# Kernel tuning notes

Measured on AMD Instinct MI355X. Metric: run time of the kernel, lower is better.

Reference implementation:

```python
import jax, jax.numpy as jnp
import numpy as np

D_MODEL = 768
NUM_HEADS = 12
HEAD_DIM = D_MODEL // NUM_HEADS  # 64, also rotary dim
INTERMEDIATE = 1152
WINDOW = 128          # config.local_attention (layer_id=1 -> local layer)
ROPE_BASE = 10000.0   # local_rope_theta
EPS = 1e-5


def layer_norm_nocenter(x, gamma):
    # keras LayerNormalization(center=False): mean-subtract, no beta
    mu = jnp.mean(x, axis=-1, keepdims=True)
    var = jnp.var(x, axis=-1, keepdims=True)
    return (x - mu) * jax.lax.rsqrt(var + EPS) * gamma


def rotate_half(x):
    x1, x2 = jnp.split(x, 2, axis=-1)
    return jnp.concatenate([-x2, x1], axis=-1)


def setup_inputs() -> dict:
    key = jax.random.key(0)
    ks = jax.random.split(key, 7)
    B, S = 4, 2048
    hidden_states = jax.random.normal(ks[0], (B, S, D_MODEL), dtype=jnp.float32)
    attention_mask = jnp.zeros((B, 1, S, S), dtype=jnp.float32)  # no padding
    s = 0.02
    attn_norm_gamma = jnp.ones((D_MODEL,), dtype=jnp.float32)
    wqkv = jax.random.normal(ks[1], (D_MODEL, 3 * D_MODEL), dtype=jnp.float32) * s
    wo_attn = jax.random.normal(ks[2], (D_MODEL, D_MODEL), dtype=jnp.float32) * s
    mlp_norm_gamma = jnp.ones((D_MODEL,), dtype=jnp.float32)
    wi = jax.random.normal(ks[3], (D_MODEL, 2 * INTERMEDIATE), dtype=jnp.float32) * s
    wo_mlp = jax.random.normal(ks[4], (INTERMEDIATE, D_MODEL), dtype=jnp.float32) * s
    return {
        'hidden_states': hidden_states,
        'attention_mask': attention_mask,
        'attn_norm_gamma': attn_norm_gamma,
        'wqkv': wqkv,
        'wo_attn': wo_attn,
        'mlp_norm_gamma': mlp_norm_gamma,
        'wi': wi,
        'wo_mlp': wo_mlp,
    }


def reference(hidden_states, attention_mask, attn_norm_gamma, wqkv, wo_attn,
              mlp_norm_gamma, wi, wo_mlp):
    B, S, Dm = hidden_states.shape
    H, Dh = NUM_HEADS, HEAD_DIM

    # RoPE cache (NTKScaling with scaling_factor=1 -> plain RoPE)
    idx = jnp.arange(0, Dh, 2, dtype=jnp.float32)
    inv_freq = 1.0 / (ROPE_BASE ** (idx / Dh))          # [Dh/2]
    t = jnp.arange(S, dtype=jnp.float32)
    freqs = t[:, None] * inv_freq[None, :]              # [S, Dh/2]
    emb = jnp.concatenate([freqs, freqs], axis=-1)      # [S, Dh]
    cos = jnp.cos(emb)[None, None]                      # [1,1,S,Dh]
    sin = jnp.sin(emb)[None, None]

    # combined sliding-window + padding mask
    pos = jnp.arange(S)
    dist = jnp.abs(pos[:, None] - pos[None, :])
    neg = jnp.finfo(jnp.float32).min
    local = jnp.where(dist <= WINDOW // 2, 0.0, neg).astype(jnp.float32)
    mask = attention_mask + local[None, None]           # [B,1,S,S]

    # attention (layer_id != 0 -> pre-norm)
    x = layer_norm_nocenter(hidden_states, attn_norm_gamma)
    qkv = (x @ wqkv).reshape(B, S, 3, H, Dh).transpose(2, 0, 3, 1, 4)
    q, k, v = qkv[0], qkv[1], qkv[2]                    # [B,H,S,Dh]
    q = q * cos + rotate_half(q) * sin
    k = k * cos + rotate_half(k) * sin

    scale = 1.0 / jnp.sqrt(jnp.asarray(Dh, q.dtype))
    scores = jnp.einsum('bhqd,bhkd->bhqk', q, k) * scale + mask
    attn = jax.nn.softmax(scores, axis=-1)
    ctx = jnp.einsum('bhqk,bhkd->bhqd', attn, v)
    attn_out = ctx.transpose(0, 2, 1, 3).reshape(B, S, Dm) @ wo_attn

    h = hidden_states + attn_out

    # GLU MLP: Wi -> split -> gelu(x)*gate -> Wo, residual
    n = layer_norm_nocenter(h, mlp_norm_gamma)
    x_in, gate = jnp.split(n @ wi, 2, axis=-1)
    mlp = jax.nn.gelu(x_in, approximate=False) * gate
    return h + mlp @ wo_mlp
```

## Files before the change

kernel.cpp:

```cpp
#include <hip/hip_runtime.h>
#include <cstdint>
#include <cstddef>

typedef __bf16 bf16;
typedef float f32x4 __attribute__((ext_vector_type(4)));
typedef __bf16 bf16x8 __attribute__((ext_vector_type(8)));
typedef __bf16 bf16x4 __attribute__((ext_vector_type(4)));
typedef __bf16 bf16x2 __attribute__((ext_vector_type(2)));

#define MFMA16(a, b, c) __builtin_amdgcn_mfma_f32_16x16x32_bf16((a), (b), (c), 0, 0, 0)

__device__ __forceinline__ void gload_lds16(const void* g, void* l) {
  __builtin_amdgcn_global_load_lds((__attribute__((address_space(1))) void*)g,
                                   (__attribute__((address_space(3))) void*)l,
                                   16, 0, 0);
}

__global__ __launch_bounds__(256) void wconv_ln(const float* __restrict__ wqkv,
                                                const float* __restrict__ woa,
                                                const float* __restrict__ wi,
                                                const float* __restrict__ wom,
                                                bf16* __restrict__ wqkvT,
                                                bf16* __restrict__ woaT,
                                                bf16* __restrict__ wiT,
                                                bf16* __restrict__ womT,
                                                const float* __restrict__ X,
                                                const float* __restrict__ gamma,
                                                bf16* __restrict__ xnout) {
  __shared__ float tile[32][33];
  const int t = threadIdx.x;
  int id = blockIdx.x;
  if (id >= 4896) {
    const int row = id - 4896;
    const float* xr = X + (size_t)row * 768;
    float v0 = xr[t], v1 = xr[t + 256], v2 = xr[t + 512];
    float s = v0 + v1 + v2;
    float s2 = v0 * v0 + v1 * v1 + v2 * v2;
#pragma unroll
    for (int m = 1; m <= 32; m <<= 1) {
      s += __shfl_xor(s, m, 64);
      s2 += __shfl_xor(s2, m, 64);
    }
    float* red = &tile[0][0];
    const int w = t >> 6, lane = t & 63;
    if (lane == 0) { red[w] = s; red[4 + w] = s2; }
    __syncthreads();
    s = red[0] + red[1] + red[2] + red[3];
    s2 = red[4] + red[5] + red[6] + red[7];
    const float mu = s * (1.f / 768.f);
    const float var = s2 * (1.f / 768.f) - mu * mu;
    const float rs = rsqrtf(var + 1e-5f);
    xnout[(size_t)row * 768 + t] = (bf16)((v0 - mu) * rs * gamma[t]);
    xnout[(size_t)row * 768 + t + 256] = (bf16)((v1 - mu) * rs * gamma[t + 256]);
    xnout[(size_t)row * 768 + t + 512] = (bf16)((v2 - mu) * rs * gamma[t + 512]);
    return;
  }
  const float* W;
  bf16* Wt;
  int K, N, bx, by;
  if (id < 1728) { W = wqkv; Wt = wqkvT; K = 768; N = 2304; bx = id % 72; by = id / 72; }
  else if (id < 2304) { id -= 1728; W = woa; Wt = woaT; K = 768; N = 768; bx = id % 24; by = id / 24; }
  else if (id < 4032) { id -= 2304; W = wi; Wt = wiT; K = 768; N = 2304; bx = id % 72; by = id / 72; }
  else { id -= 4032; W = wom; Wt = womT; K = 1152; N = 768; bx = id % 24; by = id / 24; }
  const int n0 = bx * 32, k0 = by * 32;
  const int c = t & 31, r = t >> 5;
#pragma unroll
  for (int i = 0; i < 4; ++i)
    tile[r + i * 8][c] = W[(size_t)(k0 + r + i * 8) * N + n0 + c];
  __syncthreads();
#pragma unroll
  for (int i = 0; i < 4; ++i)
    Wt[(size_t)(n0 + r + i * 8) * K + k0 + c] = (bf16)tile[c][r + i * 8];
}

__global__ __launch_bounds__(256) void ln_kernel(const float* __restrict__ X,
                                                 const float* __restrict__ gamma,
                                                 bf16* __restrict__ out) {
  const int row = blockIdx.x, t = threadIdx.x;
  const float* xr = X + (size_t)row * 768;
  float v0 = xr[t], v1 = xr[t + 256], v2 = xr[t + 512];
  float s = v0 + v1 + v2;
  float s2 = v0 * v0 + v1 * v1 + v2 * v2;
#pragma unroll
  for (int m = 1; m <= 32; m <<= 1) {
    s += __shfl_xor(s, m, 64);
    s2 += __shfl_xor(s2, m, 64);
  }
  __shared__ float red[8];
  const int w = t >> 6, lane = t & 63;
  if (lane == 0) { red[w] = s; red[4 + w] = s2; }
  __syncthreads();
  s = red[0] + red[1] + red[2] + red[3];
  s2 = red[4] + red[5] + red[6] + red[7];
  const float mu = s * (1.f / 768.f);
  const float var = s2 * (1.f / 768.f) - mu * mu;
  const float rs = rsqrtf(var + 1e-5f);
  out[(size_t)row * 768 + t] = (bf16)((v0 - mu) * rs * gamma[t]);
  out[(size_t)row * 768 + t + 256] = (bf16)((v1 - mu) * rs * gamma[t + 256]);
  out[(size_t)row * 768 + t + 512] = (bf16)((v2 - mu) * rs * gamma[t + 512]);
}

template <int BM, bool RES, typename TOUT>
__global__ __launch_bounds__(256) void gemm_bt(const bf16* __restrict__ A,
                                               const bf16* __restrict__ Bt,
                                               const float* __restrict__ Res,
                                               TOUT* __restrict__ C, int M, int N, int K) {
  constexpr int MT = BM / 32;
  __shared__ __align__(16) bf16 As[BM * 64];
  __shared__ __align__(16) bf16 Bs[128 * 64];
  const int t = threadIdx.x;
  const int lane = t & 63;
  const int w = t >> 6;
  const int wm = w >> 1, wn = w & 1;
  const int row0 = blockIdx.x * BM, col0 = blockIdx.y * 128;
  const int rm = lane & 15, qd = lane >> 4;
  f32x4 acc[MT][4] = {};
  for (int k0 = 0; k0 < K; k0 += 64) {
#pragma unroll
    for (int i = 0; i < BM / 32; ++i) {
      int c = i * 256 + t;
      int r = c >> 3, j = (c & 7) ^ (r & 7);
      gload_lds16(A + (size_t)(row0 + r) * K + (k0 + j * 8), &As[c * 8]);
    }
#pragma unroll
    for (int i = 0; i < 4; ++i) {
      int c = i * 256 + t;
      int r = c >> 3, j = (c & 7) ^ (r & 7);
      gload_lds16(Bt + (size_t)(col0 + r) * K + (k0 + j * 8), &Bs[c * 8]);
    }
    __syncthreads();
#pragma unroll
    for (int kb = 0; kb < 2; ++kb) {
      bf16x8 af[MT], bfr[4];
#pragma unroll
      for (int mt = 0; mt < MT; ++mt) {
        int r = wm * (MT * 16) + mt * 16 + rm;
        af[mt] = *(const bf16x8*)&As[r * 64 + (((kb * 4 + qd) ^ (r & 7)) * 8)];
      }
#pragma unroll
      for (int nt = 0; nt < 4; ++nt) {
        int r = wn * 64 + nt * 16 + rm;
        bfr[nt] = *(const bf16x8*)&Bs[r * 64 + (((kb * 4 + qd) ^ (r & 7)) * 8)];
      }
#pragma unroll
      for (int mt = 0; mt < MT; ++mt)
#pragma unroll
        for (int nt = 0; nt < 4; ++nt)
          acc[mt][nt] = MFMA16(af[mt], bfr[nt], acc[mt][nt]);
    }
    __syncthreads();
  }
#pragma unroll
  for (int mt = 0; mt < MT; ++mt)
#pragma unroll
    for (int nt = 0; nt < 4; ++nt) {
      const int gc = col0 + wn * 64 + nt * 16 + rm;
#pragma unroll
      for (int r = 0; r < 4; ++r) {
        const int gr = row0 + wm * (MT * 16) + mt * 16 + qd * 4 + r;
        float v = acc[mt][nt][r];
        const size_t idx = (size_t)gr * N + gc;
        if (RES) v += Res[idx];
        C[idx] = (TOUT)v;
      }
    }
}

__global__ __launch_bounds__(256) void gemm_qkv(const bf16* __restrict__ A,
                                                const bf16* __restrict__ Bt,
                                                bf16* __restrict__ Qb,
                                                bf16* __restrict__ Kb,
                                                bf16* __restrict__ Vt) {
  __shared__ __align__(16) bf16 SM[17408];
  bf16* As = SM;
  bf16* Bs = SM + 8192;

  const int t = threadIdx.x;
  const int lane = t & 63;
  const int w = t >> 6;
  const int wm = w >> 1, wn = w & 1;
  const int row0 = blockIdx.x * 128, col0 = blockIdx.y * 128;
  const int rm = lane & 15, qd = lane >> 4;
  f32x4 acc[4][4] = {};
  for (int k0 = 0; k0 < 768; k0 += 64) {
#pragma unroll
    for (int i = 0; i < 4; ++i) {
      int c = i * 256 + t;
      int r = c >> 3, j = (c & 7) ^ (r & 7);
      gload_lds16(A + (size_t)(row0 + r) * 768 + (k0 + j * 8), &As[c * 8]);
      gload_lds16(Bt + (size_t)(col0 + r) * 768 + (k0 + j * 8), &Bs[c * 8]);
    }
    __syncthreads();
#pragma unroll
    for (int kb = 0; kb < 2; ++kb) {
      bf16x8 af[4], bfr[4];
#pragma unroll
      for (int mt = 0; mt < 4; ++mt) {
        int r = wm * 64 + mt * 16 + rm;
        af[mt] = *(const bf16x8*)&As[r * 64 + (((kb * 4 + qd) ^ (r & 7)) * 8)];
      }
#pragma unroll
      for (int nt = 0; nt < 4; ++nt) {
        int r = wn * 64 + nt * 16 + rm;
        bfr[nt] = *(const bf16x8*)&Bs[r * 64 + (((kb * 4 + qd) ^ (r & 7)) * 8)];
      }
#pragma unroll
      for (int mt = 0; mt < 4; ++mt)
#pragma unroll
        for (int nt = 0; nt < 4; ++nt)
          acc[mt][nt] = MFMA16(af[mt], bfr[nt], acc[mt][nt]);
    }
    __syncthreads();
  }

  const int head_id = blockIdx.y * 2 + wn;
  const int typ = blockIdx.y / 6;
  const int b = row0 >> 11;
  const int sblk = row0 & 2047;
  const int sw = sblk + wm * 64;

  if (typ < 2) {
    const int h = head_id - typ * 12;
    const size_t bhbase = (size_t)(b * 12 + h) * 2048;
    bf16* dst = typ ? Kb : Qb;
    constexpr float inv2pi = 0.15915494309189535f;
#pragma unroll
    for (int nt = 0; nt < 2; ++nt) {
      const int d = nt * 16 + rm;
      const float invf = exp2f((float)d * -0.41524101186092029f);
      float rev = (float)(sw + qd * 4) * invf * inv2pi;
      rev -= floorf(rev);
      float cs = __builtin_amdgcn_cosf(rev);
      float sn = __builtin_amdgcn_sinf(rev);
      float rv1 = invf * inv2pi;
      float c1 = __builtin_amdgcn_cosf(rv1), s1 = __builtin_amdgcn_sinf(rv1);
      float rv13 = 13.f * invf * inv2pi;
      rv13 -= floorf(rv13);
      float c13 = __builtin_amdgcn_cosf(rv13), s13 = __builtin_amdgcn_sinf(rv13);
#pragma unroll
      for (int mt = 0; mt < 4; ++mt)
#pragma unroll
        for (int r = 0; r < 4; ++r) {
          const int s = sw + mt * 16 + qd * 4 + r;
          const float x1 = acc[mt][nt][r], x2 = acc[mt][nt + 2][r];
          bf16x2 v2;
          v2[0] = (bf16)(x1 * cs - x2 * sn);
          v2[1] = (bf16)(x2 * cs + x1 * sn);
          *(bf16x2*)&dst[(bhbase + s) * 64 + 2 * d] = v2;
          const float ca = (r < 3) ? c1 : c13, sa = (r < 3) ? s1 : s13;
          const float cn = cs * ca - sn * sa;
          sn = sn * ca + cs * sa;
          cs = cn;
        }
    }
  } else {
#pragma unroll
    for (int mt = 0; mt < 4; ++mt)
#pragma unroll
      for (int nt = 0; nt < 4; ++nt) {
        int hd = wn * 64 + nt * 16 + rm;
        int sl = wm * 64 + mt * 16 + qd * 4;
        bf16x4 v4;
#pragma unroll
        for (int r = 0; r < 4; ++r) v4[r] = (bf16)acc[mt][nt][r];
        *(bf16x4*)&SM[hd * 136 + sl] = v4;
      }
    __syncthreads();
    const int h0 = blockIdx.y * 2 - 24;
#pragma unroll
    for (int it = 0; it < 8; ++it) {
      int cc = it * 256 + t;
      int hd = cc >> 4, s8 = (cc & 15) * 8;
      bf16x8 vv = *(const bf16x8*)&SM[hd * 136 + s8];
      size_t grow = (size_t)(b * 12 + h0 + (hd >> 6)) * 64 + (hd & 63);
      *(bf16x8*)&Vt[grow * 2048 + sblk + s8] = vv;
    }
  }
}

__global__ __launch_bounds__(256) void attn_kernel(const bf16* __restrict__ Qb,
                                                   const bf16* __restrict__ Kb,
                                                   const bf16* __restrict__ Vt,
                                                   const float* __restrict__ am,
                                                   bf16* __restrict__ ctx) {
  __shared__ __align__(16) bf16 KP[64 * 200];
  __shared__ __align__(16) bf16 Vts[64 * 192];
  bf16* Ks = KP;
  bf16* Ps = KP;

  const int t = threadIdx.x;
  const int lane = t & 63, w = t >> 6;
  const int rm = lane & 15, qd = lane >> 4;
  const int s0 = blockIdx.x * 64;
  const int bh = blockIdx.y;
  const int b = bh / 12, h = bh - b * 12;
  const size_t baseQ = (size_t)bh * 2048;

#pragma unroll
  for (int i = 0; i < 6; ++i) {
    int c = i * 256 + t;
    int r = c >> 3, j = (c & 7) ^ (r & 7);
    int key = min(max(s0 - 64 + r, 0), 2047);
    gload_lds16(Kb + (baseQ + key) * 64 + j * 8, &Ks[c * 8]);
  }
#pragma unroll
  for (int i = 0; i < 6; ++i) {
    int c = i * 256 + t;
    int r = c / 24, jl = c - r * 24;
    int j = (jl & 24) | ((jl & 7) ^ (r & 7));
    int k0 = min(max(s0 - 64 + j * 8, 0), 2040);
    gload_lds16(Vt + ((size_t)bh * 64 + r) * 2048 + k0, &Vts[c * 8]);
  }

  bf16x8 aq[2];
#pragma unroll
  for (int kb = 0; kb < 2; ++kb)
    aq[kb] = *(const bf16x8*)&Qb[(baseQ + s0 + w * 16 + rm) * 64 + kb * 32 + qd * 8];

  float msk[12][4];
#pragma unroll
  for (int nt = 0; nt < 12; ++nt) {
    int key = s0 - 64 + nt * 16 + rm;
#pragma unroll
    for (int r = 0; r < 4; ++r) {
      int qpos = s0 + w * 16 + qd * 4 + r;
      bool valid = (key >= 0) && (key < 2048) && (key - qpos <= 64) && (qpos - key <= 64);
      msk[nt][r] = valid ? am[((size_t)b * 2048 + qpos) * 2048 + key] : -3e38f;
    }
  }
  __syncthreads();

  f32x4 sc[12];
#pragma unroll
  for (int nt = 0; nt < 12; ++nt) {
    f32x4 a = {0.f, 0.f, 0.f, 0.f};
#pragma unroll
    for (int kb = 0; kb < 2; ++kb) {
      int r = nt * 16 + rm;
      bf16x8 bk = *(const bf16x8*)&Ks[r * 64 + (((kb * 4 + qd) ^ (rm & 7)) * 8)];
      a = MFMA16(aq[kb], bk, a);
    }
    sc[nt] = a;
  }

  float mx[4] = {-3e38f, -3e38f, -3e38f, -3e38f};
#pragma unroll
  for (int nt = 0; nt < 12; ++nt)
#pragma unroll
    for (int r = 0; r < 4; ++r) {
      float v = (msk[nt][r] <= -2.9e38f) ? -3e38f : sc[nt][r] * 0.125f + msk[nt][r];
      sc[nt][r] = v;
      mx[r] = fmaxf(mx[r], v);
    }
#pragma unroll
  for (int r = 0; r < 4; ++r)
#pragma unroll
    for (int m = 1; m <= 8; m <<= 1) mx[r] = fmaxf(mx[r], __shfl_xor(mx[r], m, 64));
  float sum[4] = {0.f, 0.f, 0.f, 0.f};
#pragma unroll
  for (int nt = 0; nt < 12; ++nt)
#pragma unroll
    for (int r = 0; r < 4; ++r) {
      float p = (sc[nt][r] > -1e37f) ? __expf(sc[nt][r] - mx[r]) : 0.f;
      sc[nt][r] = p;
      sum[r] += p;
    }
#pragma unroll
  for (int r = 0; r < 4; ++r)
#pragma unroll
    for (int m = 1; m <= 8; m <<= 1) sum[r] += __shfl_xor(sum[r], m, 64);
  float inv[4];
#pragma unroll
  for (int r = 0; r < 4; ++r) inv[r] = 1.f / sum[r];

  __syncthreads();

#pragma unroll
  for (int nt = 0; nt < 12; ++nt)
#pragma unroll
    for (int r = 0; r < 4; ++r)
      Ps[(w * 16 + qd * 4 + r) * 200 + nt * 16 + rm] = (bf16)(sc[nt][r] * inv[r]);

  f32x4 o[4] = {};
#pragma unroll
  for (int ks = 0; ks < 6; ++ks) {
    bf16x8 ap = *(const bf16x8*)&Ps[(w * 16 + rm) * 200 + ks * 32 + qd * 8];
#pragma unroll
    for (int nt = 0; nt < 4; ++nt) {
      int kc = ks * 4 + qd;
      bf16x8 bv = *(const bf16x8*)&Vts[(nt * 16 + rm) * 192 +
                                       (((kc & 24) | ((kc & 7) ^ (rm & 7))) * 8)];
      o[nt] = MFMA16(ap, bv, o[nt]);
    }
  }
#pragma unroll
  for (int nt = 0; nt < 4; ++nt)
#pragma unroll
    for (int r = 0; r < 4; ++r) {
      int q_ = s0 + w * 16 + qd * 4 + r;
      ctx[((size_t)(b * 2048 + q_)) * 768 + h * 64 + nt * 16 + rm] = (bf16)o[nt][r];
    }
}

__global__ __launch_bounds__(128) void geglu_kernel(const bf16* __restrict__ X,
                                                    bf16* __restrict__ out) {
  const int row = blockIdx.y;
  const int c = blockIdx.x * 128 + threadIdx.x;
  const bf16* xr = X + (size_t)row * 2304;
  float x = (float)xr[c], g = (float)xr[1152 + c];
  float ge = 0.5f * x * (1.0f + erff(x * 0.70710678118654752f));
  out[(size_t)row * 1152 + c] = (bf16)(ge * g);
}

extern "C" void kernel_launch(void* const* d_in, const int* in_sizes, int n_in,
                              void* d_out, int out_size, void* d_ws, size_t ws_size,
                              hipStream_t stream) {
  (void)in_sizes; (void)n_in; (void)out_size; (void)ws_size;
  const float* hidden = (const float*)d_in[0];
  const float* amask = (const float*)d_in[1];
  const float* g1 = (const float*)d_in[2];
  const float* wqkv = (const float*)d_in[3];
  const float* woa = (const float*)d_in[4];
  const float* g2 = (const float*)d_in[5];
  const float* wi = (const float*)d_in[6];
  const float* wom = (const float*)d_in[7];
  float* out = (float*)d_out;

  char* p = (char*)d_ws;
  size_t o = 0;
  auto take = [&](size_t bytes) {
    char* r = p + o;
    o = (o + bytes + 255) & ~(size_t)255;
    return r;
  };
  bf16* wqkvT = (bf16*)take((size_t)2304 * 768 * 2);
  bf16* woaT = (bf16*)take((size_t)768 * 768 * 2);
  bf16* wiT = (bf16*)take((size_t)2304 * 768 * 2);
  bf16* womT = (bf16*)take((size_t)768 * 1152 * 2);
  bf16* xn = (bf16*)take((size_t)8192 * 768 * 2);
  bf16* Qb = (bf16*)take((size_t)98304 * 64 * 2);
  bf16* Kb = (bf16*)take((size_t)98304 * 64 * 2);
  bf16* Vt = (bf16*)take((size_t)98304 * 64 * 2);
  bf16* ctxb = (bf16*)take((size_t)8192 * 768 * 2);
  float* hbuf = (float*)take((size_t)8192 * 768 * 4);
  bf16* mlpx = (bf16*)take((size_t)8192 * 2304 * 2);
  bf16* mlp = (bf16*)take((size_t)8192 * 1152 * 2);

  wconv_ln<<<13088, 256, 0, stream>>>(wqkv, woa, wi, wom, wqkvT, woaT, wiT, womT,
                                      hidden, g1, xn);

  gemm_qkv<<<dim3(64, 18), 256, 0, stream>>>(xn, wqkvT, Qb, Kb, Vt);
  attn_kernel<<<dim3(32, 48), 256, 0, stream>>>(Qb, Kb, Vt, amask, ctxb);
  gemm_bt<64, true, float><<<dim3(128, 6), 256, 0, stream>>>(ctxb, woaT, hidden, hbuf,
                                                             8192, 768, 768);

  ln_kernel<<<8192, 256, 0, stream>>>(hbuf, g2, xn);
  gemm_bt<128, false, bf16><<<dim3(64, 18), 256, 0, stream>>>(xn, wiT, nullptr, mlpx,
                                                              8192, 2304, 768);
  geglu_kernel<<<dim3(9, 8192), 128, 0, stream>>>(mlpx, mlp);
  gemm_bt<64, true, float><<<dim3(128, 6), 256, 0, stream>>>(mlp, womT, hbuf, out,
                                                             8192, 768, 1152);
}
```

Measured before the change: 326.4 us.

## Double-buffer GEMMs with 256-row tiles and fuse GEGLU into Wi GEMM epilogue

All GEMMs move to 512-thread blocks with 256x128 tiles and a double-buffered LDS pipeline that prefetches the next k-tiles with async global-to-LDS loads while MFMAs run, using explicit waitcnt, barriers and setprio. The Wi GEMM interleaves the x and gate weight rows so each block holds matching columns, applying GELU*gate in the epilogue and removing the separate geglu kernel and its intermediate buffer. The goal is to hide load latency and cut memory traffic. The cost is higher LDS use per block, fewer blocks for the narrow GEMMs (192 blocks), and hand-counted vmcnt values that must stay correct.

```diff
diff --git a/kernel.cpp b/kernel.cpp
--- a/kernel.cpp
+++ b/kernel.cpp
@@ -100,121 +100,155 @@
   out[(size_t)row * 768 + t + 512] = (bf16)((v2 - mu) * rs * gamma[t + 512]);
 }
 
-template <int BM, bool RES, typename TOUT>
-__global__ __launch_bounds__(256) void gemm_bt(const bf16* __restrict__ A,
-                                               const bf16* __restrict__ Bt,
-                                               const float* __restrict__ Res,
-                                               TOUT* __restrict__ C, int M, int N, int K) {
-  constexpr int MT = BM / 32;
-  __shared__ __align__(16) bf16 As[BM * 64];
-  __shared__ __align__(16) bf16 Bs[128 * 64];
+#define GEMM_CORE_LOOP(NT_, AROW_EXPR, BROW_EXPR)                                   \
+  auto stage = [&](int tile) {                                                      \
+    const int kk0 = tile * 64;                                                      \
+    bf16* Ab_ = &SM[(tile & 1) * 24576];                                            \
+    bf16* Bb_ = Ab_ + 16384;                                                        \
+    _Pragma("unroll") for (int i = 0; i < 4; ++i) {                                 \
+      int c = i * 512 + t;                                                          \
+      int r = c >> 3, j = (c & 7) ^ (r & 7);                                        \
+      gload_lds16(Ap + (size_t)(AROW_EXPR) * Kd + (kk0 + j * 8), &Ab_[c * 8]);      \
+    }                                                                               \
+    _Pragma("unroll") for (int i = 0; i < 2; ++i) {                                 \
+      int c = i * 512 + t;                                                          \
+      int r = c >> 3, j = (c & 7) ^ (r & 7);                                        \
+      gload_lds16(Bp + (size_t)(BROW_EXPR) * Kd + (kk0 + j * 8), &Bb_[c * 8]);      \
+    }                                                                               \
+  };                                                                                \
+  stage(0);                                                                         \
+  stage(1);                                                                         \
+  asm volatile("s_waitcnt vmcnt(6)" ::: "memory");                                  \
+  __builtin_amdgcn_s_barrier();                                                     \
+  __builtin_amdgcn_sched_barrier(0);                                                \
+  for (int tt = 0; tt < NT_; ++tt) {                                                \
+    const bf16* Ab = &SM[(tt & 1) * 24576];                                         \
+    const bf16* Bb = Ab + 16384;                                                    \
+    bf16x8 af[4], bfr[4];                                                           \
+                                                                \
+    _Pragma("unroll") for (int mt = 0; mt < 4; ++mt) {                              \
+      int r = wm * 64 + mt * 16 + rm;                                               \
+      af[mt] = *(const bf16x8*)&Ab[r * 64 + ((qd ^ (r & 7)) * 8)];                  \
+    }                                                                               \
+    _Pragma("unroll") for (int nt = 0; nt < 4; ++nt) {                              \
+      int r = wn * 64 + nt * 16 + rm;                                               \
+      bfr[nt] = *(const bf16x8*)&Bb[r * 64 + ((qd ^ (r & 7)) * 8)];                 \
+    }                                                                               \
+    __builtin_amdgcn_s_barrier();                                                   \
+    __builtin_amdgcn_sched_barrier(0);                                              \
+    __builtin_amdgcn_s_setprio(1);                                                  \
+    _Pragma("unroll") for (int mt = 0; mt < 4; ++mt)                                \
+        _Pragma("unroll") for (int nt = 0; nt < 4; ++nt)                            \
+            acc[mt][nt] = MFMA16(af[mt], bfr[nt], acc[mt][nt]);                     \
+    __builtin_amdgcn_s_setprio(0);                                                  \
+    __builtin_amdgcn_s_barrier();                                                   \
+    __builtin_amdgcn_sched_barrier(0);                                              \
+                                                                \
+    _Pragma("unroll") for (int mt = 0; mt < 4; ++mt) {                              \
+      int r = wm * 64 + mt * 16 + rm;                                               \
+      af[mt] = *(const bf16x8*)&Ab[r * 64 + (((4 + qd) ^ (r & 7)) * 8)];            \
+    }                                                                               \
+    _Pragma("unroll") for (int nt = 0; nt < 4; ++nt) {                              \
+      int r = wn * 64 + nt * 16 + rm;                                               \
+      bfr[nt] = *(const bf16x8*)&Bb[r * 64 + (((4 + qd) ^ (r & 7)) * 8)];           \
+    }                                                                               \
+    asm volatile("s_waitcnt lgkmcnt(0)" ::: "memory");                              \
+    __builtin_amdgcn_sched_barrier(0);                                              \
+    __builtin_amdgcn_s_barrier();           \
+    __builtin_amdgcn_sched_barrier(0);                                              \
+    if (tt + 2 < NT_) stage(tt + 2);                                                \
+    __builtin_amdgcn_s_setprio(1);                                                  \
+    _Pragma("unroll") for (int mt = 0; mt < 4; ++mt)                                \
+        _Pragma("unroll") for (int nt = 0; nt < 4; ++nt)                            \
+            acc[mt][nt] = MFMA16(af[mt], bfr[nt], acc[mt][nt]);                     \
+    __builtin_amdgcn_s_setprio(0);                                                  \
+    if (tt + 2 < NT_) {                                                             \
+      asm volatile("s_waitcnt vmcnt(6)" ::: "memory");                              \
+    } else {                                                                        \
+      asm volatile("s_waitcnt vmcnt(0)" ::: "memory");                              \
+    }                                                                               \
+    __builtin_amdgcn_s_barrier();                                                   \
+    __builtin_amdgcn_sched_barrier(0);                                              \
+  }
+
+template <int EPI, int NT>
+__global__ __launch_bounds__(512, 2) void gemm_big(const bf16* __restrict__ Ap,
+                                                   const bf16* __restrict__ Bp,
+                                                   const float* __restrict__ Res,
+                                                   void* __restrict__ Cout,
+                                                   int Nout) {
+  constexpr int Kd = NT * 64;
+  __shared__ __align__(16) bf16 SM[49152];
   const int t = threadIdx.x;
-  const int lane = t & 63;
-  const int w = t >> 6;
+  const int lane = t & 63, w = t >> 6;
   const int wm = w >> 1, wn = w & 1;
-  const int row0 = blockIdx.x * BM, col0 = blockIdx.y * 128;
   const int rm = lane & 15, qd = lane >> 4;
-  f32x4 acc[MT][4] = {};
-  for (int k0 = 0; k0 < K; k0 += 64) {
-#pragma unroll
-    for (int i = 0; i < BM / 32; ++i) {
-      int c = i * 256 + t;
-      int r = c >> 3, j = (c & 7) ^ (r & 7);
-      gload_lds16(A + (size_t)(row0 + r) * K + (k0 + j * 8), &As[c * 8]);
-    }
-#pragma unroll
-    for (int i = 0; i < 4; ++i) {
-      int c = i * 256 + t;
-      int r = c >> 3, j = (c & 7) ^ (r & 7);
-      gload_lds16(Bt + (size_t)(col0 + r) * K + (k0 + j * 8), &Bs[c * 8]);
-    }
-    __syncthreads();
-#pragma unroll
-    for (int kb = 0; kb < 2; ++kb) {
-      bf16x8 af[MT], bfr[4];
-#pragma unroll
-      for (int mt = 0; mt < MT; ++mt) {
-        int r = wm * (MT * 16) + mt * 16 + rm;
-        af[mt] = *(const bf16x8*)&As[r * 64 + (((kb * 4 + qd) ^ (r & 7)) * 8)];
+  const int by = blockIdx.y;
+  const int row0 = blockIdx.x * 256;
+  f32x4 acc[4][4] = {};
+
+  auto brow = [&](int r) -> int {
+    if constexpr (EPI == 1) {
+      int q = (r >> 4) & 3;
+      return ((q & 1) ? 1152 : 0) + by * 64 + (r >> 6) * 32 + ((q >> 1) << 4) + (r & 15);
+    } else {
+      return by * 128 + r;
+    }
+  };
+
+  GEMM_CORE_LOOP(NT, row0 + r, brow(r))
+
+  if constexpr (EPI == 0) {
+    float* C = (float*)Cout;
+#pragma unroll
+    for (int mt = 0; mt < 4; ++mt)
+#pragma unroll
+      for (int nt = 0; nt < 4; ++nt) {
+        const int gc = by * 128 + wn * 64 + nt * 16 + rm;
+#pragma unroll
+        for (int r = 0; r < 4; ++r) {
+          const int gr = row0 + wm * 64 + mt * 16 + qd * 4 + r;
+          const size_t idx = (size_t)gr * Nout + gc;
+          C[idx] = Res[idx] + acc[mt][nt][r];
+        }
       }
-#pragma unroll
-      for (int nt = 0; nt < 4; ++nt) {
-        int r = wn * 64 + nt * 16 + rm;
-        bfr[nt] = *(const bf16x8*)&Bs[r * 64 + (((kb * 4 + qd) ^ (r & 7)) * 8)];
+  } else {
+    bf16* C = (bf16*)Cout;
+#pragma unroll
+    for (int mt = 0; mt < 4; ++mt)
+#pragma unroll
+      for (int g = 0; g < 2; ++g) {
+        const int gc = by * 64 + wn * 32 + g * 16 + rm;
+#pragma unroll
+        for (int r = 0; r < 4; ++r) {
+          const int gr = row0 + wm * 64 + mt * 16 + qd * 4 + r;
+          const float x = acc[mt][g * 2][r], gv = acc[mt][g * 2 + 1][r];
+          const float ge = 0.5f * x * (1.0f + erff(x * 0.70710678118654752f));
+          C[(size_t)gr * 1152 + gc] = (bf16)(ge * gv);
+        }
       }
-#pragma unroll
-      for (int mt = 0; mt < MT; ++mt)
-#pragma unroll
-        for (int nt = 0; nt < 4; ++nt)
-          acc[mt][nt] = MFMA16(af[mt], bfr[nt], acc[mt][nt]);
-    }
-    __syncthreads();
-  }
-#pragma unroll
-  for (int mt = 0; mt < MT; ++mt)
-#pragma unroll
-    for (int nt = 0; nt < 4; ++nt) {
-      const int gc = col0 + wn * 64 + nt * 16 + rm;
-#pragma unroll
-      for (int r = 0; r < 4; ++r) {
-        const int gr = row0 + wm * (MT * 16) + mt * 16 + qd * 4 + r;
-        float v = acc[mt][nt][r];
-        const size_t idx = (size_t)gr * N + gc;
-        if (RES) v += Res[idx];
-        C[idx] = (TOUT)v;
-      }
-    }
-}
-
-__global__ __launch_bounds__(256) void gemm_qkv(const bf16* __restrict__ A,
-                                                const bf16* __restrict__ Bt,
-                                                bf16* __restrict__ Qb,
-                                                bf16* __restrict__ Kb,
-                                                bf16* __restrict__ Vt) {
-  __shared__ __align__(16) bf16 SM[17408];
-  bf16* As = SM;
-  bf16* Bs = SM + 8192;
-
+  }
+}
+
+__global__ __launch_bounds__(512, 2) void gemm_qkv2(const bf16* __restrict__ Ap,
+                                                    const bf16* __restrict__ Bp,
+                                                    bf16* __restrict__ Qb,
+                                                    bf16* __restrict__ Kb,
+                                                    bf16* __restrict__ Vt) {
+  constexpr int Kd = 768;
+  __shared__ __align__(16) bf16 SM[49152];
   const int t = threadIdx.x;
-  const int lane = t & 63;
-  const int w = t >> 6;
+  const int lane = t & 63, w = t >> 6;
   const int wm = w >> 1, wn = w & 1;
-  const int row0 = blockIdx.x * 128, col0 = blockIdx.y * 128;
   const int rm = lane & 15, qd = lane >> 4;
+  const int by = blockIdx.y;
+  const int row0 = blockIdx.x * 256;
   f32x4 acc[4][4] = {};
-  for (int k0 = 0; k0 < 768; k0 += 64) {
-#pragma unroll
-    for (int i = 0; i < 4; ++i) {
-      int c = i * 256 + t;
-      int r = c >> 3, j = (c & 7) ^ (r & 7);
-      gload_lds16(A + (size_t)(row0 + r) * 768 + (k0 + j * 8), &As[c * 8]);
-      gload_lds16(Bt + (size_t)(col0 + r) * 768 + (k0 + j * 8), &Bs[c * 8]);
-    }
-    __syncthreads();
-#pragma unroll
-    for (int kb = 0; kb < 2; ++kb) {
-      bf16x8 af[4], bfr[4];
-#pragma unroll
-      for (int mt = 0; mt < 4; ++mt) {
-        int r = wm * 64 + mt * 16 + rm;
-        af[mt] = *(const bf16x8*)&As[r * 64 + (((kb * 4 + qd) ^ (r & 7)) * 8)];
-      }
-#pragma unroll
-      for (int nt = 0; nt < 4; ++nt) {
-        int r = wn * 64 + nt * 16 + rm;
-        bfr[nt] = *(const bf16x8*)&Bs[r * 64 + (((kb * 4 + qd) ^ (r & 7)) * 8)];
-      }
-#pragma unroll
-      for (int mt = 0; mt < 4; ++mt)
-#pragma unroll
-        for (int nt = 0; nt < 4; ++nt)
-          acc[mt][nt] = MFMA16(af[mt], bfr[nt], acc[mt][nt]);
-    }
-    __syncthreads();
-  }
-
-  const int head_id = blockIdx.y * 2 + wn;
-  const int typ = blockIdx.y / 6;
+
+  GEMM_CORE_LOOP(12, row0 + r, by * 128 + r)
+
+  const int head_id = by * 2 + wn;
+  const int typ = by / 6;
   const int b = row0 >> 11;
   const int sblk = row0 & 2047;
   const int sw = sblk + wm * 64;
@@ -263,15 +297,15 @@
         bf16x4 v4;
 #pragma unroll
         for (int r = 0; r < 4; ++r) v4[r] = (bf16)acc[mt][nt][r];
-        *(bf16x4*)&SM[hd * 136 + sl] = v4;
+        *(bf16x4*)&SM[hd * 264 + sl] = v4;
       }
     __syncthreads();
-    const int h0 = blockIdx.y * 2 - 24;
+    const int h0 = by * 2 - 24;
 #pragma unroll
     for (int it = 0; it < 8; ++it) {
-      int cc = it * 256 + t;
-      int hd = cc >> 4, s8 = (cc & 15) * 8;
-      bf16x8 vv = *(const bf16x8*)&SM[hd * 136 + s8];
+      int cc = it * 512 + t;
+      int hd = cc >> 5, s8 = (cc & 31) * 8;
+      bf16x8 vv = *(const bf16x8*)&SM[hd * 264 + s8];
       size_t grow = (size_t)(b * 12 + h0 + (hd >> 6)) * 64 + (hd & 63);
       *(bf16x8*)&Vt[grow * 2048 + sblk + s8] = vv;
     }
@@ -400,16 +434,6 @@
       int q_ = s0 + w * 16 + qd * 4 + r;
       ctx[((size_t)(b * 2048 + q_)) * 768 + h * 64 + nt * 16 + rm] = (bf16)o[nt][r];
     }
-}
-
-__global__ __launch_bounds__(128) void geglu_kernel(const bf16* __restrict__ X,
-                                                    bf16* __restrict__ out) {
-  const int row = blockIdx.y;
-  const int c = blockIdx.x * 128 + threadIdx.x;
-  const bf16* xr = X + (size_t)row * 2304;
-  float x = (float)xr[c], g = (float)xr[1152 + c];
-  float ge = 0.5f * x * (1.0f + erff(x * 0.70710678118654752f));
-  out[(size_t)row * 1152 + c] = (bf16)(ge * g);
 }
 
 extern "C" void kernel_launch(void* const* d_in, const int* in_sizes, int n_in,
@@ -443,21 +467,16 @@
   bf16* Vt = (bf16*)take((size_t)98304 * 64 * 2);
   bf16* ctxb = (bf16*)take((size_t)8192 * 768 * 2);
   float* hbuf = (float*)take((size_t)8192 * 768 * 4);
-  bf16* mlpx = (bf16*)take((size_t)8192 * 2304 * 2);
   bf16* mlp = (bf16*)take((size_t)8192 * 1152 * 2);
 
   wconv_ln<<<13088, 256, 0, stream>>>(wqkv, woa, wi, wom, wqkvT, woaT, wiT, womT,
                                       hidden, g1, xn);
 
-  gemm_qkv<<<dim3(64, 18), 256, 0, stream>>>(xn, wqkvT, Qb, Kb, Vt);
+  gemm_qkv2<<<dim3(32, 18), 512, 0, stream>>>(xn, wqkvT, Qb, Kb, Vt);
   attn_kernel<<<dim3(32, 48), 256, 0, stream>>>(Qb, Kb, Vt, amask, ctxb);
-  gemm_bt<64, true, float><<<dim3(128, 6), 256, 0, stream>>>(ctxb, woaT, hidden, hbuf,
-                                                             8192, 768, 768);
+  gemm_big<0, 12><<<dim3(32, 6), 512, 0, stream>>>(ctxb, woaT, hidden, hbuf, 768);
 
   ln_kernel<<<8192, 256, 0, stream>>>(hbuf, g2, xn);
-  gemm_bt<128, false, bf16><<<dim3(64, 18), 256, 0, stream>>>(xn, wiT, nullptr, mlpx,
-                                                              8192, 2304, 768);
-  geglu_kernel<<<dim3(9, 8192), 128, 0, stream>>>(mlpx, mlp);
-  gemm_bt<64, true, float><<<dim3(128, 6), 256, 0, stream>>>(mlp, womT, hbuf, out,
-                                                             8192, 768, 1152);
-}
+  gemm_big<1, 12><<<dim3(32, 18), 512, 0, stream>>>(xn, wiT, nullptr, mlp, 1152);
+  gemm_big<0, 18><<<dim3(32, 6), 512, 0, stream>>>(mlp, womT, hbuf, out, 768);
+}
```

After: 307.8 us. 1.06x faster.
